# Optimization experiments

Measured on AMD Instinct MI355X. Metric: run time of the kernel, lower is better.

## Reference

```python
import jax, jax.numpy as jnp
import numpy as np

D = 768

def _cdist(a, b):
    # Euclidean pairwise distance like torch.cdist(p=2).
    sq_a = jnp.sum(a * a, axis=1)
    sq_b = jnp.sum(b * b, axis=1)
    d2 = sq_a[:, None] + sq_b[None, :] - 2.0 * (a @ b.T)
    return jnp.sqrt(jnp.maximum(d2, 1e-12))  # clamp kills sqrt(0) issues on the diagonal


def setup_inputs() -> dict:
    key = jax.random.key(0)
    k1, k2, k3, k4 = jax.random.split(key, 4)
    image_feature = jax.random.normal(k1, (1, 4096, D), dtype=jnp.float32)
    bank = jax.random.normal(k2, (8192, D), dtype=jnp.float32)
    # HGNN params (two hypergraph conv layers, n_hid=1024), eval mode (dropout off)
    w1 = jax.random.normal(k3, (D, 1024), dtype=jnp.float32) * (1.0 / np.sqrt(D))
    b1 = jnp.zeros((1024,), dtype=jnp.float32)
    w2 = jax.random.normal(k4, (1024, D), dtype=jnp.float32) * (1.0 / np.sqrt(1024))
    b2 = jnp.zeros((D,), dtype=jnp.float32)
    return {"image_feature": image_feature, "bank": bank,
            "w1": w1, "b1": b1, "w2": w2, "b2": b2}


def reference(image_feature, bank, w1, b1, w2, b2):
    n = image_feature.shape[1]  # feature_number
    nodes = jnp.concatenate([image_feature.reshape(-1, D), bank.reshape(-1, D)], axis=0)
    # full pairwise cdist over all nodes (image + bank), as in the original
    adj = 1.0 / (1.0 + _cdist(nodes, nodes))  # [N_total, N_total]
    score_map = adj[:n, :n]
    # top-2 per row; index of the 2nd-highest similarity (nearest non-self neighbor)
    _, idx_top2 = jax.lax.top_k(score_map, 2)
    index = idx_top2[:, 1]                     # [n] int32
    pseudo_features = jnp.take(nodes, index, axis=0)  # gather [n, D]
    # HGNN: x = G @ (relu(G @ (x W1 + b1)) W2 + b2), dropout=0 (eval)
    x = nodes[:n]
    G = score_map
    h = jax.nn.relu(G @ (x @ w1 + b1))
    out = G @ (h @ w2 + b2)
    return out, pseudo_features
```

## Files before the change

kernel.cpp:

```cpp
#include <hip/hip_runtime.h>

typedef unsigned short u16;
typedef unsigned int u32;
typedef signed char i8s;
typedef __attribute__((ext_vector_type(8))) short bf16x8;
typedef __attribute__((ext_vector_type(4))) float f32x4;
typedef __attribute__((ext_vector_type(4))) int i32x4;

#define NT 4096
#define DD 768
#define HH 1024

#define MU 0.0249f
#define GD 0.999999f
#define SDELTA 42000.0f
#define ST 16.0f

__device__ __forceinline__ u16 f2bf(float f) {
  union { float f; unsigned u; } v; v.f = f;
  return (u16)((v.u + 0x7fffu + ((v.u >> 16) & 1u)) >> 16);
}
__device__ __forceinline__ float bf2f(u16 b) {
  union { u32 u; float f; } v; v.u = (u32)b << 16; return v.f;
}

__device__ __forceinline__ void async16(const void* g, void* l) {
  __builtin_amdgcn_global_load_lds(
      (const __attribute__((address_space(1))) void*)g,
      (__attribute__((address_space(3))) void*)l, 16, 0, 0);
}


__device__ __forceinline__ void trans32(const float* __restrict__ src,
                                        u16* __restrict__ dst, int R, int C,
                                        int bx, int by, u16 tile[32][33]) {
  int c0 = bx * 32, r0 = by * 32;
  int tx = threadIdx.x & 31, ty = threadIdx.x >> 5;
#pragma unroll
  for (int i = 0; i < 32; i += 8)
    tile[ty + i][tx] = f2bf(src[(size_t)(r0 + ty + i) * C + c0 + tx]);
  __syncthreads();
#pragma unroll
  for (int i = 0; i < 32; i += 8)
    dst[(size_t)(c0 + ty + i) * R + r0 + tx] = tile[tx][ty + i];
}

__global__ __launch_bounds__(256) void prep_all(
    const float* __restrict__ X, u16* __restrict__ Xb, float* __restrict__ sq,
    const float* __restrict__ w1, u16* __restrict__ w1t,
    const float* __restrict__ w2, u16* __restrict__ w2t,
    float* __restrict__ csum1, float* __restrict__ csum2) {
  __shared__ float red[256];
  __shared__ u16 tile[32][33];
  int b = blockIdx.x, t = threadIdx.x;
  if (b < NT) {
    const float* xr = X + (size_t)b * DD;
    float a = 0.f;
    for (int i = t; i < DD; i += 256) {
      float v = xr[i];
      Xb[(size_t)b * DD + i] = f2bf(v);
      a += v * v;
    }
    red[t] = a;
    __syncthreads();
    for (int s = 128; s > 0; s >>= 1) {
      if (t < s) red[t] += red[t + s];
      __syncthreads();
    }
    if (t == 0) sq[b] = red[0];
  } else if (b < NT + 768) {
    int idx = b - NT;
    trans32(w1, w1t, DD, HH, idx & 31, idx >> 5, tile);
  } else if (b < NT + 1536) {
    int idx = b - NT - 768;
    trans32(w2, w2t, HH, DD, idx % 24, idx / 24, tile);
  } else {
    for (int i = t; i < HH; i += 256) csum1[i] = 0.f;
    for (int i = t; i < DD; i += 256) csum2[i] = 0.f;
  }
}


__global__ __launch_bounds__(256) void gemm_sym_i8(
    const u16* __restrict__ Xb, const float* __restrict__ sq,
    i8s* __restrict__ Dq) {
  __shared__ __attribute__((aligned(16))) u16 As[128 * 64];
  __shared__ __attribute__((aligned(16))) u16 Bs[64 * 64];
  int t = blockIdx.x, by = 0;
  while (t >= 64 - 2 * by) { t -= 64 - 2 * by; ++by; }
  const int bx = 2 * by + t;
  const int tid = threadIdx.x;
  const int wave = tid >> 6, lane = tid & 63;
  const int quad = lane >> 4, l16 = lane & 15;
  const int wm = wave >> 1, wn = wave & 1;
  const int row0 = by * 128, col0 = bx * 64;

  f32x4 acc[4][2];
#pragma unroll
  for (int i = 0; i < 4; ++i)
#pragma unroll
    for (int j = 0; j < 2; ++j) acc[i][j] = (f32x4){0.f, 0.f, 0.f, 0.f};

  for (int kt = 0; kt < DD; kt += 64) {
#pragma unroll
    for (int it = 0; it < 4; ++it) {
      int c = it * 256 + tid;
      int r = c >> 3, sc = c & 7;
      int gch = sc ^ (r & 7);
      async16(Xb + (size_t)(row0 + r) * DD + kt + gch * 8, As + (size_t)c * 8);
    }
#pragma unroll
    for (int it = 0; it < 2; ++it) {
      int c = it * 256 + tid;
      int r = c >> 3, sc = c & 7;
      int gch = sc ^ (r & 7);
      async16(Xb + (size_t)(col0 + r) * DD + kt + gch * 8, Bs + (size_t)c * 8);
    }
    __syncthreads();
#pragma unroll
    for (int ks = 0; ks < 2; ++ks) {
      const int sl = (ks * 4 + quad) ^ (l16 & 7);
      bf16x8 af[4], bfr[2];
#pragma unroll
      for (int tt = 0; tt < 4; ++tt)
        af[tt] = *(const bf16x8*)(As + (wm * 64 + tt * 16 + l16) * 64 + sl * 8);
#pragma unroll
      for (int u = 0; u < 2; ++u)
        bfr[u] = *(const bf16x8*)(Bs + (wn * 32 + u * 16 + l16) * 64 + sl * 8);
#pragma unroll
      for (int tm = 0; tm < 4; ++tm)
#pragma unroll
        for (int tn = 0; tn < 2; ++tn)
          acc[tm][tn] = __builtin_amdgcn_mfma_f32_16x16x32_bf16(af[tm], bfr[tn], acc[tm][tn], 0, 0, 0);
    }
    __syncthreads();
  }

  i8s* Ls = (i8s*)As;
#pragma unroll
  for (int tm = 0; tm < 4; ++tm) {
    const int li0 = wm * 64 + tm * 16 + quad * 4;
    const int gi0 = row0 + li0;
#pragma unroll
    for (int tn = 0; tn < 2; ++tn) {
      const int lj = wn * 32 + tn * 16 + l16;
      const int gj = col0 + lj;
      const float sqj = sq[gj];
      u32 mpack = 0;
#pragma unroll
      for (int r = 0; r < 4; ++r) {
        const int gi = gi0 + r;
        float d2 = fmaxf(sq[gi] + sqj - 2.f * acc[tm][tn][r], 1e-12f);
        float g = __builtin_amdgcn_rcpf(1.f + __builtin_amdgcn_sqrtf(d2));
        int q = __float2int_rn((g - MU) * SDELTA);
        q = min(max(q, -127), 127);
        if (gi == gj) q = 0;
        Ls[(li0 + r) * 64 + lj] = (i8s)q;
        mpack |= ((u32)(unsigned char)(i8s)q) << (r * 8);
      }
      if (gj > gi0 + 3)
        *(u32*)(Dq + (size_t)gj * NT + gi0) = mpack;
    }
  }
  __syncthreads();
#pragma unroll
  for (int it = 0; it < 2; ++it) {
    int s = it * 256 + tid;
    int r = s >> 2, ch = s & 3;
    *(uint4*)(Dq + (size_t)(row0 + r) * NT + col0 + ch * 16) = *(const uint4*)(Ls + s * 16);
  }
}


__global__ __launch_bounds__(256) void gemm_btq(
    const u16* __restrict__ A, const u16* __restrict__ B,
    int M, int N, int K,
    const float* __restrict__ bias, u16* __restrict__ Crow,
    i8s* __restrict__ Tq, float* __restrict__ csum) {
  __shared__ __attribute__((aligned(16))) u16 As[128 * 64];
  __shared__ __attribute__((aligned(16))) u16 Bs[64 * 64];
  const int tid = threadIdx.x;
  const int wave = tid >> 6, lane = tid & 63;
  const int quad = lane >> 4, l16 = lane & 15;
  const int wm = wave >> 1, wn = wave & 1;
  const int row0 = blockIdx.y * 128, col0 = blockIdx.x * 64;

  f32x4 acc[4][2];
#pragma unroll
  for (int i = 0; i < 4; ++i)
#pragma unroll
    for (int j = 0; j < 2; ++j) acc[i][j] = (f32x4){0.f, 0.f, 0.f, 0.f};

  for (int kt = 0; kt < K; kt += 64) {
#pragma unroll
    for (int it = 0; it < 4; ++it) {
      int c = it * 256 + tid;
      int r = c >> 3, sc = c & 7;
      int gch = sc ^ (r & 7);
      async16(A + (size_t)(row0 + r) * K + kt + gch * 8, As + (size_t)c * 8);
    }
#pragma unroll
    for (int it = 0; it < 2; ++it) {
      int c = it * 256 + tid;
      int r = c >> 3, sc = c & 7;
      int gch = sc ^ (r & 7);
      async16(B + (size_t)(col0 + r) * K + kt + gch * 8, Bs + (size_t)c * 8);
    }
    __syncthreads();
#pragma unroll
    for (int ks = 0; ks < 2; ++ks) {
      const int sl = (ks * 4 + quad) ^ (l16 & 7);
      bf16x8 af[4], bfr[2];
#pragma unroll
      for (int tt = 0; tt < 4; ++tt)
        af[tt] = *(const bf16x8*)(As + (wm * 64 + tt * 16 + l16) * 64 + sl * 8);
#pragma unroll
      for (int u = 0; u < 2; ++u)
        bfr[u] = *(const bf16x8*)(Bs + (wn * 32 + u * 16 + l16) * 64 + sl * 8);
#pragma unroll
      for (int tm = 0; tm < 4; ++tm)
#pragma unroll
        for (int tn = 0; tn < 2; ++tn)
          acc[tm][tn] = __builtin_amdgcn_mfma_f32_16x16x32_bf16(af[tm], bfr[tn], acc[tm][tn], 0, 0, 0);
    }
    __syncthreads();
  }

#pragma unroll
  for (int tm = 0; tm < 4; ++tm) {
    const int gi0 = row0 + wm * 64 + tm * 16 + quad * 4;
#pragma unroll
    for (int r = 0; r < 4; ++r) {
      const int gi = gi0 + r;
      const float b = bias[gi];
      float rowsum = 0.f;
#pragma unroll
      for (int tn = 0; tn < 2; ++tn) {
        const int gj = col0 + wn * 32 + tn * 16 + l16;
        u16 hb = f2bf(acc[tm][tn][r] + b);
        float f = bf2f(hb);
        Crow[(size_t)gi * N + gj] = hb;
        int q = __float2int_rn(f * ST);
        q = min(max(q, -127), 127);
        Tq[(size_t)gi * N + gj] = (i8s)q;
        rowsum += f;
      }
#pragma unroll
      for (int off = 1; off < 16; off <<= 1) rowsum += __shfl_xor(rowsum, off);
      if (l16 == 0) atomicAdd(csum + gi, rowsum);
    }
  }
}


template <int EPI>
__global__ __launch_bounds__(256) void gemm_i8(
    const i8s* __restrict__ Aq, const i8s* __restrict__ Bq,
    const u16* __restrict__ Tt, const float* __restrict__ csum,
    int N, float inv, u16* __restrict__ Hout, float* __restrict__ Fout) {
  __shared__ __attribute__((aligned(16))) char lds[49152];
  i8s* As = (i8s*)lds;
  i8s* Bs = (i8s*)(lds + 32768);
  const int tid = threadIdx.x;
  const int wave = tid >> 6, lane = tid & 63;
  const int quad = lane >> 4, l16 = lane & 15;
  const int wm = wave >> 1, wn = wave & 1;
  const int id = blockIdx.y * gridDim.x + blockIdx.x;
  const int mm = id >> 3;
  const int by = (id & 7) * 4 + (mm & 3);
  const int bx = mm >> 2;
  const int row0 = by * 128, col0 = bx * 64;

  i32x4 acc[4][2];
#pragma unroll
  for (int i = 0; i < 4; ++i)
#pragma unroll
    for (int j = 0; j < 2; ++j) acc[i][j] = (i32x4){0, 0, 0, 0};

  for (int kt = 0; kt < NT; kt += 256) {
#pragma unroll
    for (int it = 0; it < 8; ++it) {
      int c = it * 256 + tid;
      int r = c >> 4, sc = c & 15;
      int gch = (sc & 8) | ((sc & 7) ^ (r & 7));
      async16(Aq + (size_t)(row0 + r) * NT + kt + gch * 16, As + (size_t)c * 16);
    }
#pragma unroll
    for (int it = 0; it < 4; ++it) {
      int c = it * 256 + tid;
      int r = c >> 4, sc = c & 15;
      int gch = (sc & 8) | ((sc & 7) ^ (r & 7));
      async16(Bq + (size_t)(col0 + r) * NT + kt + gch * 16, Bs + (size_t)c * 16);
    }
    __syncthreads();
#pragma unroll
    for (int ks = 0; ks < 4; ++ks) {
      const int ch = ks * 4 + quad;
      const int sl = (ch & 8) | ((ch & 7) ^ (l16 & 7));
      i32x4 af[4], bfr[2];
#pragma unroll
      for (int t = 0; t < 4; ++t)
        af[t] = *(const i32x4*)(As + (wm * 64 + t * 16 + l16) * 256 + sl * 16);
#pragma unroll
      for (int u = 0; u < 2; ++u)
        bfr[u] = *(const i32x4*)(Bs + (wn * 32 + u * 16 + l16) * 256 + sl * 16);
#pragma unroll
      for (int tm = 0; tm < 4; ++tm)
#pragma unroll
        for (int tn = 0; tn < 2; ++tn)
          acc[tm][tn] = __builtin_amdgcn_mfma_i32_16x16x64_i8(af[tm], bfr[tn], acc[tm][tn], 0, 0, 0);
    }
    __syncthreads();
  }

  u16* Tl = (u16*)lds;
  {
    int r = tid >> 2, cseg = (tid & 3) * 32;
    const u16* src = Tt + (size_t)(col0 + r) * NT + row0 + cseg;
    u16* dst = Tl + r * 136 + cseg;
#pragma unroll
    for (int q = 0; q < 4; ++q)
      *(uint4*)(dst + q * 8) = *(const uint4*)(src + q * 8);
  }
  __syncthreads();

#pragma unroll
  for (int tm = 0; tm < 4; ++tm) {
    const int gi0 = row0 + wm * 64 + tm * 16 + quad * 4;
#pragma unroll
    for (int tn = 0; tn < 2; ++tn) {
      const int gj = col0 + wn * 32 + tn * 16 + l16;
      const float cs = csum[gj];
#pragma unroll
      for (int r = 0; r < 4; ++r) {
        const int gi = gi0 + r;
        float tv = bf2f(Tl[(gj - col0) * 136 + (gi - row0)]);
        float v = (float)acc[tm][tn][r] * inv + MU * cs + (GD - MU) * tv;
        if constexpr (EPI == 0)
          Hout[(size_t)gi * N + gj] = f2bf(fmaxf(v, 0.f));
        else
          Fout[(size_t)gi * N + gj] = v;
      }
    }
  }
}


__global__ __launch_bounds__(256) void topk_rerank(
    const i8s* __restrict__ Dq, const float* __restrict__ X,
    const float* __restrict__ sq, float* __restrict__ outP) {
  __shared__ u32 wtop[4][8];
  __shared__ int idx8[8];
  __shared__ float dv[8];
  __shared__ int dj[8];
  __shared__ int jstar;
  int row = blockIdx.x, t = threadIdx.x;
  int wave = t >> 6, lane = t & 63;

  const uint4 v = *(const uint4*)(Dq + (size_t)row * NT + t * 16);
  u32 w[4] = {v.x, v.y, v.z, v.w};
  u32 k0 = 0xFFFFFFFFu, k1 = 0xFFFFFFFFu, k2 = 0xFFFFFFFFu, k3 = 0xFFFFFFFFu;
#pragma unroll
  for (int e = 0; e < 16; ++e) {
    int q = (int)(i8s)((w[e >> 2] >> ((e & 3) * 8)) & 0xFFu);
    u32 key = ((u32)(127 - q) << 16) | (u32)(t * 16 + e);
    if (key < k3) {
      if (key < k2) { k3 = k2;
        if (key < k1) { k2 = k1;
          if (key < k0) { k1 = k0; k0 = key; } else k1 = key;
        } else k2 = key;
      } else k3 = key;
    }
  }
  u32 loc[4] = {k0, k1, k2, k3};
  int head = 0;
  for (int rr = 0; rr < 8; ++rr) {
    u32 k = (head < 4) ? loc[head] : 0xFFFFFFFFu;
    u32 m = k;
#pragma unroll
    for (int off = 32; off > 0; off >>= 1) {
      u32 o = (u32)__shfl_xor((int)m, off);
      if (o < m) m = o;
    }
    if (k == m) ++head;
    if (lane == 0) wtop[wave][rr] = m;
  }
  __syncthreads();
  if (wave == 0) {
    u32 k = (lane < 32) ? wtop[lane >> 3][lane & 7] : 0xFFFFFFFFu;
    for (int rr = 0; rr < 8; ++rr) {
      u32 m = k;
#pragma unroll
      for (int off = 32; off > 0; off >>= 1) {
        u32 o = (u32)__shfl_xor((int)m, off);
        if (o < m) m = o;
      }
      if (k == m) k = 0xFFFFFFFFu;
      if (lane == 0) idx8[rr] = (int)(m & 0xFFFFu);
    }
  }
  __syncthreads();

  const float* xi = X + (size_t)row * DD;
  for (int p = wave; p < 8; p += 4) {
    int j = idx8[p];
    const float* xj = X + (size_t)j * DD;
    float s = 0.f;
#pragma unroll
    for (int tt = 0; tt < DD / 64; ++tt) {
      int k = lane + tt * 64;
      s += xi[k] * xj[k];
    }
    for (int off = 32; off > 0; off >>= 1) s += __shfl_down(s, off);
    if (lane == 0) {
      dv[p] = sq[row] + sq[j] - 2.f * s;
      dj[p] = j;
    }
  }
  __syncthreads();
  if (t == 0) {
    float bd = dv[0]; int bj = dj[0];
    for (int c = 1; c < 8; ++c)
      if (dv[c] < bd || (dv[c] == bd && dj[c] < bj)) { bd = dv[c]; bj = dj[c]; }
    jstar = bj;
  }
  __syncthreads();
  const float* xs = X + (size_t)jstar * DD;
  for (int k = t; k < DD; k += 256) outP[(size_t)row * DD + k] = xs[k];
}


extern "C" void kernel_launch(void* const* d_in, const int* in_sizes, int n_in,
                              void* d_out, int out_size, void* d_ws, size_t ws_size,
                              hipStream_t stream) {
  const float* X  = (const float*)d_in[0];
  const float* w1 = (const float*)d_in[2];
  const float* b1 = (const float*)d_in[3];
  const float* w2 = (const float*)d_in[4];
  const float* b2 = (const float*)d_in[5];
  float* out = (float*)d_out;

  char* p = (char*)d_ws;
  auto carve = [&](size_t bytes) {
    char* r = p;
    p += (bytes + 255) & ~(size_t)255;
    return (void*)r;
  };
  u16*   Xb    = (u16*)carve((size_t)NT * DD * 2);
  u16*   w1t   = (u16*)carve((size_t)HH * DD * 2);
  u16*   w2t   = (u16*)carve((size_t)DD * HH * 2);
  float* sq    = (float*)carve((size_t)NT * 4);
  i8s*   Dq    = (i8s*)carve((size_t)NT * NT);
  u16*   T1t   = (u16*)carve((size_t)HH * NT * 2);
  i8s*   T1q   = (i8s*)carve((size_t)HH * NT);
  float* csum1 = (float*)carve((size_t)HH * 4);
  u16*   Hm    = (u16*)carve((size_t)NT * HH * 2);
  u16*   T2t   = (u16*)carve((size_t)DD * NT * 2);
  i8s*   T2q   = (i8s*)carve((size_t)DD * NT);
  float* csum2 = (float*)carve((size_t)DD * 4);

  const float inv1 = 1.0f / (SDELTA * ST);

  prep_all<<<NT + 768 + 768 + 1, 256, 0, stream>>>(
      X, Xb, sq, w1, w1t, w2, w2t, csum1, csum2);

  gemm_sym_i8<<<1056, 256, 0, stream>>>(Xb, sq, Dq);

  gemm_btq<<<dim3(NT / 64, HH / 128), 256, 0, stream>>>(
      w1t, Xb, HH, NT, DD, b1, T1t, T1q, csum1);

  gemm_i8<0><<<dim3(HH / 64, NT / 128), 256, 0, stream>>>(
      Dq, T1q, T1t, csum1, HH, inv1, Hm, nullptr);

  gemm_btq<<<dim3(NT / 64, DD / 128), 256, 0, stream>>>(
      w2t, Hm, DD, NT, HH, b2, T2t, T2q, csum2);

  gemm_i8<1><<<dim3(DD / 64, NT / 128), 256, 0, stream>>>(
      Dq, T2q, T2t, csum2, DD, inv1, nullptr, out);

  topk_rerank<<<NT, 256, 0, stream>>>(Dq, X, sq, out + (size_t)NT * DD);
}
```

Baseline: 268.7 us.

## Merge independent kernels into combined launches to fill idle CUs

Regroups the seven launches into five by putting independent work in one grid with a blockIdx split. The first W1 GEMM runs with the symmetric distance GEMM, the top-k candidate search runs with the first int8 propagation GEMM, the rerank runs with the W2 GEMM, and the final gather runs with the last int8 GEMM. Small GEMM grids (384–512 blocks) underfill the GPU, and the aim is to fill the tail with the per-row top-k work and save launch gaps. In exchange, candidate and index arrays now go through global memory, and each merged kernel reserves the larger LDS size for every block, which may lower occupancy of the lighter blocks.

```diff
diff --git a/kernel.cpp b/kernel.cpp
--- a/kernel.cpp
+++ b/kernel.cpp
@@ -81,11 +81,188 @@
 }
 
 
-__global__ __launch_bounds__(256) void gemm_sym_i8(
+__device__ __forceinline__ void btq_tile(
+    const u16* __restrict__ A, const u16* __restrict__ B,
+    int N, int K, const float* __restrict__ bias,
+    u16* __restrict__ Crow, i8s* __restrict__ Tq, float* __restrict__ csum,
+    int row0, int col0, u16* As, u16* Bs) {
+  const int tid = threadIdx.x;
+  const int wave = tid >> 6, lane = tid & 63;
+  const int quad = lane >> 4, l16 = lane & 15;
+  const int wm = wave >> 1, wn = wave & 1;
+
+  f32x4 acc[4][2];
+#pragma unroll
+  for (int i = 0; i < 4; ++i)
+#pragma unroll
+    for (int j = 0; j < 2; ++j) acc[i][j] = (f32x4){0.f, 0.f, 0.f, 0.f};
+
+  for (int kt = 0; kt < K; kt += 64) {
+#pragma unroll
+    for (int it = 0; it < 4; ++it) {
+      int c = it * 256 + tid;
+      int r = c >> 3, sc = c & 7;
+      int gch = sc ^ (r & 7);
+      async16(A + (size_t)(row0 + r) * K + kt + gch * 8, As + (size_t)c * 8);
+    }
+#pragma unroll
+    for (int it = 0; it < 2; ++it) {
+      int c = it * 256 + tid;
+      int r = c >> 3, sc = c & 7;
+      int gch = sc ^ (r & 7);
+      async16(B + (size_t)(col0 + r) * K + kt + gch * 8, Bs + (size_t)c * 8);
+    }
+    __syncthreads();
+#pragma unroll
+    for (int ks = 0; ks < 2; ++ks) {
+      const int sl = (ks * 4 + quad) ^ (l16 & 7);
+      bf16x8 af[4], bfr[2];
+#pragma unroll
+      for (int tt = 0; tt < 4; ++tt)
+        af[tt] = *(const bf16x8*)(As + (wm * 64 + tt * 16 + l16) * 64 + sl * 8);
+#pragma unroll
+      for (int u = 0; u < 2; ++u)
+        bfr[u] = *(const bf16x8*)(Bs + (wn * 32 + u * 16 + l16) * 64 + sl * 8);
+#pragma unroll
+      for (int tm = 0; tm < 4; ++tm)
+#pragma unroll
+        for (int tn = 0; tn < 2; ++tn)
+          acc[tm][tn] = __builtin_amdgcn_mfma_f32_16x16x32_bf16(af[tm], bfr[tn], acc[tm][tn], 0, 0, 0);
+    }
+    __syncthreads();
+  }
+
+#pragma unroll
+  for (int tm = 0; tm < 4; ++tm) {
+    const int gi0 = row0 + wm * 64 + tm * 16 + quad * 4;
+#pragma unroll
+    for (int r = 0; r < 4; ++r) {
+      const int gi = gi0 + r;
+      const float b = bias[gi];
+      float rowsum = 0.f;
+#pragma unroll
+      for (int tn = 0; tn < 2; ++tn) {
+        const int gj = col0 + wn * 32 + tn * 16 + l16;
+        u16 hb = f2bf(acc[tm][tn][r] + b);
+        float f = bf2f(hb);
+        Crow[(size_t)gi * N + gj] = hb;
+        int q = __float2int_rn(f * ST);
+        q = min(max(q, -127), 127);
+        Tq[(size_t)gi * N + gj] = (i8s)q;
+        rowsum += f;
+      }
+#pragma unroll
+      for (int off = 1; off < 16; off <<= 1) rowsum += __shfl_xor(rowsum, off);
+      if (l16 == 0) atomicAdd(csum + gi, rowsum);
+    }
+  }
+}
+
+
+template <int EPI>
+__device__ __forceinline__ void i8_tile(
+    const i8s* __restrict__ Aq, const i8s* __restrict__ Bq,
+    const u16* __restrict__ Tt, const float* __restrict__ csum,
+    int N, float inv, u16* __restrict__ Hout, float* __restrict__ Fout,
+    int row0, int col0, char* lds) {
+  i8s* As = (i8s*)lds;
+  i8s* Bs = (i8s*)(lds + 32768);
+  const int tid = threadIdx.x;
+  const int wave = tid >> 6, lane = tid & 63;
+  const int quad = lane >> 4, l16 = lane & 15;
+  const int wm = wave >> 1, wn = wave & 1;
+
+  i32x4 acc[4][2];
+#pragma unroll
+  for (int i = 0; i < 4; ++i)
+#pragma unroll
+    for (int j = 0; j < 2; ++j) acc[i][j] = (i32x4){0, 0, 0, 0};
+
+  for (int kt = 0; kt < NT; kt += 256) {
+#pragma unroll
+    for (int it = 0; it < 8; ++it) {
+      int c = it * 256 + tid;
+      int r = c >> 4, sc = c & 15;
+      int gch = (sc & 8) | ((sc & 7) ^ (r & 7));
+      async16(Aq + (size_t)(row0 + r) * NT + kt + gch * 16, As + (size_t)c * 16);
+    }
+#pragma unroll
+    for (int it = 0; it < 4; ++it) {
+      int c = it * 256 + tid;
+      int r = c >> 4, sc = c & 15;
+      int gch = (sc & 8) | ((sc & 7) ^ (r & 7));
+      async16(Bq + (size_t)(col0 + r) * NT + kt + gch * 16, Bs + (size_t)c * 16);
+    }
+    __syncthreads();
+#pragma unroll
+    for (int ks = 0; ks < 4; ++ks) {
+      const int ch = ks * 4 + quad;
+      const int sl = (ch & 8) | ((ch & 7) ^ (l16 & 7));
+      i32x4 af[4], bfr[2];
+#pragma unroll
+      for (int t = 0; t < 4; ++t)
+        af[t] = *(const i32x4*)(As + (wm * 64 + t * 16 + l16) * 256 + sl * 16);
+#pragma unroll
+      for (int u = 0; u < 2; ++u)
+        bfr[u] = *(const i32x4*)(Bs + (wn * 32 + u * 16 + l16) * 256 + sl * 16);
+#pragma unroll
+      for (int tm = 0; tm < 4; ++tm)
+#pragma unroll
+        for (int tn = 0; tn < 2; ++tn)
+          acc[tm][tn] = __builtin_amdgcn_mfma_i32_16x16x64_i8(af[tm], bfr[tn], acc[tm][tn], 0, 0, 0);
+    }
+    __syncthreads();
+  }
+
+  u16* Tl = (u16*)lds;
+  {
+    int r = tid >> 2, cseg = (tid & 3) * 32;
+    const u16* src = Tt + (size_t)(col0 + r) * NT + row0 + cseg;
+    u16* dst = Tl + r * 136 + cseg;
+#pragma unroll
+    for (int q = 0; q < 4; ++q)
+      *(uint4*)(dst + q * 8) = *(const uint4*)(src + q * 8);
+  }
+  __syncthreads();
+
+#pragma unroll
+  for (int tm = 0; tm < 4; ++tm) {
+    const int gi0 = row0 + wm * 64 + tm * 16 + quad * 4;
+#pragma unroll
+    for (int tn = 0; tn < 2; ++tn) {
+      const int gj = col0 + wn * 32 + tn * 16 + l16;
+      const float cs = csum[gj];
+#pragma unroll
+      for (int r = 0; r < 4; ++r) {
+        const int gi = gi0 + r;
+        float tv = bf2f(Tl[(gj - col0) * 136 + (gi - row0)]);
+        float v = (float)acc[tm][tn][r] * inv + MU * cs + (GD - MU) * tv;
+        if constexpr (EPI == 0)
+          Hout[(size_t)gi * N + gj] = f2bf(fmaxf(v, 0.f));
+        else
+          Fout[(size_t)gi * N + gj] = v;
+      }
+    }
+  }
+}
+
+
+__global__ __launch_bounds__(256) void stage2(
     const u16* __restrict__ Xb, const float* __restrict__ sq,
-    i8s* __restrict__ Dq) {
-  __shared__ __attribute__((aligned(16))) u16 As[128 * 64];
-  __shared__ __attribute__((aligned(16))) u16 Bs[64 * 64];
+    i8s* __restrict__ Dq,
+    const u16* __restrict__ w1t, const float* __restrict__ b1,
+    u16* __restrict__ T1t, i8s* __restrict__ T1q, float* __restrict__ csum1) {
+  __shared__ __attribute__((aligned(16))) char lds[24576];
+  u16* As = (u16*)lds;
+  u16* Bs = (u16*)(lds + 16384);
+
+  if (blockIdx.x >= 1056) {
+    const int bid = blockIdx.x - 1056;
+    btq_tile(w1t, Xb, NT, DD, b1, T1t, T1q, csum1,
+             (bid >> 6) * 128, (bid & 63) * 64, As, Bs);
+    return;
+  }
+
   int t = blockIdx.x, by = 0;
   while (t >= 64 - 2 * by) { t -= 64 - 2 * by; ++by; }
   const int bx = 2 * by + t;
@@ -172,190 +349,26 @@
 }
 
 
-__global__ __launch_bounds__(256) void gemm_btq(
-    const u16* __restrict__ A, const u16* __restrict__ B,
-    int M, int N, int K,
-    const float* __restrict__ bias, u16* __restrict__ Crow,
-    i8s* __restrict__ Tq, float* __restrict__ csum) {
-  __shared__ __attribute__((aligned(16))) u16 As[128 * 64];
-  __shared__ __attribute__((aligned(16))) u16 Bs[64 * 64];
-  const int tid = threadIdx.x;
-  const int wave = tid >> 6, lane = tid & 63;
-  const int quad = lane >> 4, l16 = lane & 15;
-  const int wm = wave >> 1, wn = wave & 1;
-  const int row0 = blockIdx.y * 128, col0 = blockIdx.x * 64;
-
-  f32x4 acc[4][2];
-#pragma unroll
-  for (int i = 0; i < 4; ++i)
-#pragma unroll
-    for (int j = 0; j < 2; ++j) acc[i][j] = (f32x4){0.f, 0.f, 0.f, 0.f};
-
-  for (int kt = 0; kt < K; kt += 64) {
-#pragma unroll
-    for (int it = 0; it < 4; ++it) {
-      int c = it * 256 + tid;
-      int r = c >> 3, sc = c & 7;
-      int gch = sc ^ (r & 7);
-      async16(A + (size_t)(row0 + r) * K + kt + gch * 8, As + (size_t)c * 8);
-    }
-#pragma unroll
-    for (int it = 0; it < 2; ++it) {
-      int c = it * 256 + tid;
-      int r = c >> 3, sc = c & 7;
-      int gch = sc ^ (r & 7);
-      async16(B + (size_t)(col0 + r) * K + kt + gch * 8, Bs + (size_t)c * 8);
-    }
-    __syncthreads();
-#pragma unroll
-    for (int ks = 0; ks < 2; ++ks) {
-      const int sl = (ks * 4 + quad) ^ (l16 & 7);
-      bf16x8 af[4], bfr[2];
-#pragma unroll
-      for (int tt = 0; tt < 4; ++tt)
-        af[tt] = *(const bf16x8*)(As + (wm * 64 + tt * 16 + l16) * 64 + sl * 8);
-#pragma unroll
-      for (int u = 0; u < 2; ++u)
-        bfr[u] = *(const bf16x8*)(Bs + (wn * 32 + u * 16 + l16) * 64 + sl * 8);
-#pragma unroll
-      for (int tm = 0; tm < 4; ++tm)
-#pragma unroll
-        for (int tn = 0; tn < 2; ++tn)
-          acc[tm][tn] = __builtin_amdgcn_mfma_f32_16x16x32_bf16(af[tm], bfr[tn], acc[tm][tn], 0, 0, 0);
-    }
-    __syncthreads();
-  }
-
-#pragma unroll
-  for (int tm = 0; tm < 4; ++tm) {
-    const int gi0 = row0 + wm * 64 + tm * 16 + quad * 4;
-#pragma unroll
-    for (int r = 0; r < 4; ++r) {
-      const int gi = gi0 + r;
-      const float b = bias[gi];
-      float rowsum = 0.f;
-#pragma unroll
-      for (int tn = 0; tn < 2; ++tn) {
-        const int gj = col0 + wn * 32 + tn * 16 + l16;
-        u16 hb = f2bf(acc[tm][tn][r] + b);
-        float f = bf2f(hb);
-        Crow[(size_t)gi * N + gj] = hb;
-        int q = __float2int_rn(f * ST);
-        q = min(max(q, -127), 127);
-        Tq[(size_t)gi * N + gj] = (i8s)q;
-        rowsum += f;
-      }
-#pragma unroll
-      for (int off = 1; off < 16; off <<= 1) rowsum += __shfl_xor(rowsum, off);
-      if (l16 == 0) atomicAdd(csum + gi, rowsum);
-    }
-  }
-}
-
-
-template <int EPI>
-__global__ __launch_bounds__(256) void gemm_i8(
-    const i8s* __restrict__ Aq, const i8s* __restrict__ Bq,
-    const u16* __restrict__ Tt, const float* __restrict__ csum,
-    int N, float inv, u16* __restrict__ Hout, float* __restrict__ Fout) {
+__global__ __launch_bounds__(256) void stage3(
+    const i8s* __restrict__ Dq, const i8s* __restrict__ T1q,
+    const u16* __restrict__ T1t, const float* __restrict__ csum1,
+    float inv, u16* __restrict__ Hm, int* __restrict__ cand) {
   __shared__ __attribute__((aligned(16))) char lds[49152];
-  i8s* As = (i8s*)lds;
-  i8s* Bs = (i8s*)(lds + 32768);
-  const int tid = threadIdx.x;
-  const int wave = tid >> 6, lane = tid & 63;
-  const int quad = lane >> 4, l16 = lane & 15;
-  const int wm = wave >> 1, wn = wave & 1;
-  const int id = blockIdx.y * gridDim.x + blockIdx.x;
-  const int mm = id >> 3;
-  const int by = (id & 7) * 4 + (mm & 3);
-  const int bx = mm >> 2;
-  const int row0 = by * 128, col0 = bx * 64;
-
-  i32x4 acc[4][2];
-#pragma unroll
-  for (int i = 0; i < 4; ++i)
-#pragma unroll
-    for (int j = 0; j < 2; ++j) acc[i][j] = (i32x4){0, 0, 0, 0};
-
-  for (int kt = 0; kt < NT; kt += 256) {
-#pragma unroll
-    for (int it = 0; it < 8; ++it) {
-      int c = it * 256 + tid;
-      int r = c >> 4, sc = c & 15;
-      int gch = (sc & 8) | ((sc & 7) ^ (r & 7));
-      async16(Aq + (size_t)(row0 + r) * NT + kt + gch * 16, As + (size_t)c * 16);
-    }
-#pragma unroll
-    for (int it = 0; it < 4; ++it) {
-      int c = it * 256 + tid;
-      int r = c >> 4, sc = c & 15;
-      int gch = (sc & 8) | ((sc & 7) ^ (r & 7));
-      async16(Bq + (size_t)(col0 + r) * NT + kt + gch * 16, Bs + (size_t)c * 16);
-    }
-    __syncthreads();
-#pragma unroll
-    for (int ks = 0; ks < 4; ++ks) {
-      const int ch = ks * 4 + quad;
-      const int sl = (ch & 8) | ((ch & 7) ^ (l16 & 7));
-      i32x4 af[4], bfr[2];
-#pragma unroll
-      for (int t = 0; t < 4; ++t)
-        af[t] = *(const i32x4*)(As + (wm * 64 + t * 16 + l16) * 256 + sl * 16);
-#pragma unroll
-      for (int u = 0; u < 2; ++u)
-        bfr[u] = *(const i32x4*)(Bs + (wn * 32 + u * 16 + l16) * 256 + sl * 16);
-#pragma unroll
-      for (int tm = 0; tm < 4; ++tm)
-#pragma unroll
-        for (int tn = 0; tn < 2; ++tn)
-          acc[tm][tn] = __builtin_amdgcn_mfma_i32_16x16x64_i8(af[tm], bfr[tn], acc[tm][tn], 0, 0, 0);
-    }
-    __syncthreads();
-  }
-
-  u16* Tl = (u16*)lds;
-  {
-    int r = tid >> 2, cseg = (tid & 3) * 32;
-    const u16* src = Tt + (size_t)(col0 + r) * NT + row0 + cseg;
-    u16* dst = Tl + r * 136 + cseg;
-#pragma unroll
-    for (int q = 0; q < 4; ++q)
-      *(uint4*)(dst + q * 8) = *(const uint4*)(src + q * 8);
-  }
-  __syncthreads();
-
-#pragma unroll
-  for (int tm = 0; tm < 4; ++tm) {
-    const int gi0 = row0 + wm * 64 + tm * 16 + quad * 4;
-#pragma unroll
-    for (int tn = 0; tn < 2; ++tn) {
-      const int gj = col0 + wn * 32 + tn * 16 + l16;
-      const float cs = csum[gj];
-#pragma unroll
-      for (int r = 0; r < 4; ++r) {
-        const int gi = gi0 + r;
-        float tv = bf2f(Tl[(gj - col0) * 136 + (gi - row0)]);
-        float v = (float)acc[tm][tn][r] * inv + MU * cs + (GD - MU) * tv;
-        if constexpr (EPI == 0)
-          Hout[(size_t)gi * N + gj] = f2bf(fmaxf(v, 0.f));
-        else
-          Fout[(size_t)gi * N + gj] = v;
-      }
-    }
-  }
-}
-
-
-__global__ __launch_bounds__(256) void topk_rerank(
-    const i8s* __restrict__ Dq, const float* __restrict__ X,
-    const float* __restrict__ sq, float* __restrict__ outP) {
-  __shared__ u32 wtop[4][8];
-  __shared__ int idx8[8];
-  __shared__ float dv[8];
-  __shared__ int dj[8];
-  __shared__ int jstar;
-  int row = blockIdx.x, t = threadIdx.x;
-  int wave = t >> 6, lane = t & 63;
+
+  if (blockIdx.x < 512) {
+    const int id = blockIdx.x;
+    const int mm = id >> 3;
+    const int by = (id & 7) * 4 + (mm & 3);
+    const int bx = mm >> 2;
+    i8_tile<0>(Dq, T1q, T1t, csum1, HH, inv, Hm, nullptr,
+               by * 128, bx * 64, lds);
+    return;
+  }
+
+  const int row = blockIdx.x - 512;
+  const int t = threadIdx.x;
+  const int wave = t >> 6, lane = t & 63;
+  u32* wtop = (u32*)lds;
 
   const uint4 v = *(const uint4*)(Dq + (size_t)row * NT + t * 16);
   u32 w[4] = {v.x, v.y, v.z, v.w};
@@ -383,11 +396,11 @@
       if (o < m) m = o;
     }
     if (k == m) ++head;
-    if (lane == 0) wtop[wave][rr] = m;
+    if (lane == 0) wtop[wave * 8 + rr] = m;
   }
   __syncthreads();
   if (wave == 0) {
-    u32 k = (lane < 32) ? wtop[lane >> 3][lane & 7] : 0xFFFFFFFFu;
+    u32 k = (lane < 32) ? wtop[lane] : 0xFFFFFFFFu;
     for (int rr = 0; rr < 8; ++rr) {
       u32 m = k;
 #pragma unroll
@@ -396,14 +409,35 @@
         if (o < m) m = o;
       }
       if (k == m) k = 0xFFFFFFFFu;
-      if (lane == 0) idx8[rr] = (int)(m & 0xFFFFu);
-    }
-  }
-  __syncthreads();
-
+      if (lane == 0) cand[row * 8 + rr] = (int)(m & 0xFFFFu);
+    }
+  }
+}
+
+
+__global__ __launch_bounds__(256) void stage4(
+    const u16* __restrict__ w2t, const u16* __restrict__ Hm,
+    const float* __restrict__ b2, u16* __restrict__ T2t,
+    i8s* __restrict__ T2q, float* __restrict__ csum2,
+    const float* __restrict__ X, const float* __restrict__ sq,
+    const int* __restrict__ cand, int* __restrict__ jidx) {
+  __shared__ __attribute__((aligned(16))) char lds[24576];
+
+  if (blockIdx.x < 384) {
+    const int bid = blockIdx.x;
+    btq_tile(w2t, Hm, NT, HH, b2, T2t, T2q, csum2,
+             (bid >> 6) * 128, (bid & 63) * 64, (u16*)lds, (u16*)(lds + 16384));
+    return;
+  }
+
+  const int row = blockIdx.x - 384;
+  const int t = threadIdx.x;
+  const int wave = t >> 6, lane = t & 63;
+  float* dv = (float*)lds;
+  int* dj = (int*)(lds + 32);
   const float* xi = X + (size_t)row * DD;
   for (int p = wave; p < 8; p += 4) {
-    int j = idx8[p];
+    int j = cand[row * 8 + p];
     const float* xj = X + (size_t)j * DD;
     float s = 0.f;
 #pragma unroll
@@ -422,11 +456,35 @@
     float bd = dv[0]; int bj = dj[0];
     for (int c = 1; c < 8; ++c)
       if (dv[c] < bd || (dv[c] == bd && dj[c] < bj)) { bd = dv[c]; bj = dj[c]; }
-    jstar = bj;
-  }
-  __syncthreads();
-  const float* xs = X + (size_t)jstar * DD;
-  for (int k = t; k < DD; k += 256) outP[(size_t)row * DD + k] = xs[k];
+    jidx[row] = bj;
+  }
+}
+
+
+__global__ __launch_bounds__(256) void stage5(
+    const i8s* __restrict__ Dq, const i8s* __restrict__ T2q,
+    const u16* __restrict__ T2t, const float* __restrict__ csum2,
+    float inv, float* __restrict__ Fout,
+    const float* __restrict__ X, const int* __restrict__ jidx,
+    float* __restrict__ outP) {
+  __shared__ __attribute__((aligned(16))) char lds[49152];
+
+  if (blockIdx.x < 384) {
+    const int id = blockIdx.x;
+    const int mm = id >> 3;
+    const int by = (id & 7) * 4 + (mm & 3);
+    const int bx = mm >> 2;
+    i8_tile<1>(Dq, T2q, T2t, csum2, DD, inv, nullptr, Fout,
+               by * 128, bx * 64, lds);
+    return;
+  }
+
+  const int row = blockIdx.x - 384;
+  const int t = threadIdx.x;
+  const int j = jidx[row];
+  const float4* src = (const float4*)(X + (size_t)j * DD);
+  float4* dst = (float4*)(outP + (size_t)row * DD);
+  if (t < DD / 4) dst[t] = src[t];
 }
 
 
@@ -458,25 +516,21 @@
   u16*   T2t   = (u16*)carve((size_t)DD * NT * 2);
   i8s*   T2q   = (i8s*)carve((size_t)DD * NT);
   float* csum2 = (float*)carve((size_t)DD * 4);
+  int*   cand  = (int*)carve((size_t)NT * 8 * sizeof(int));
+  int*   jidx  = (int*)carve((size_t)NT * sizeof(int));
 
   const float inv1 = 1.0f / (SDELTA * ST);
 
   prep_all<<<NT + 768 + 768 + 1, 256, 0, stream>>>(
       X, Xb, sq, w1, w1t, w2, w2t, csum1, csum2);
 
-  gemm_sym_i8<<<1056, 256, 0, stream>>>(Xb, sq, Dq);
-
-  gemm_btq<<<dim3(NT / 64, HH / 128), 256, 0, stream>>>(
-      w1t, Xb, HH, NT, DD, b1, T1t, T1q, csum1);
-
-  gemm_i8<0><<<dim3(HH / 64, NT / 128), 256, 0, stream>>>(
-      Dq, T1q, T1t, csum1, HH, inv1, Hm, nullptr);
-
-  gemm_btq<<<dim3(NT / 64, DD / 128), 256, 0, stream>>>(
-      w2t, Hm, DD, NT, HH, b2, T2t, T2q, csum2);
-
-  gemm_i8<1><<<dim3(DD / 64, NT / 128), 256, 0, stream>>>(
-      Dq, T2q, T2t, csum2, DD, inv1, nullptr, out);
-
-  topk_rerank<<<NT, 256, 0, stream>>>(Dq, X, sq, out + (size_t)NT * DD);
-}
+  stage2<<<1056 + 512, 256, 0, stream>>>(Xb, sq, Dq, w1t, b1, T1t, T1q, csum1);
+
+  stage3<<<512 + NT, 256, 0, stream>>>(Dq, T1q, T1t, csum1, inv1, Hm, cand);
+
+  stage4<<<384 + NT, 256, 0, stream>>>(w2t, Hm, b2, T2t, T2q, csum2,
+                                       X, sq, cand, jidx);
+
+  stage5<<<384 + NT, 256, 0, stream>>>(Dq, T2q, T2t, csum2, inv1, out,
+                                       X, jidx, out + (size_t)NT * DD);
+}
```

After: 258.5 us. -3.8%, faster.
